# Optimization experiments

Measured on AMD Instinct MI355X. Metric: run time of the kernel, lower is better.

## Reference

```python
import jax, jax.numpy as jnp
import numpy as np

B, L, D_MODEL, D_STATE, D_CONV, EXPAND = 2, 1024, 1024, 16, 4, 2
D_INNER = D_MODEL * EXPAND


def setup_inputs() -> dict:
    key = jax.random.key(0)
    ks = jax.random.split(key, 8)
    s = lambda fan: 1.0 / np.sqrt(fan)
    x = jax.random.normal(ks[0], (B, L, D_MODEL), jnp.float32)
    in_proj_w = jax.random.normal(ks[1], (D_MODEL, 2 * D_INNER), jnp.float32) * s(D_MODEL)
    conv_w = jax.random.normal(ks[2], (D_INNER, 1, D_CONV), jnp.float32) * s(D_CONV)
    conv_b = jax.random.normal(ks[3], (D_INNER,), jnp.float32) * 0.01
    x_proj_w = jax.random.normal(ks[4], (D_INNER, 2 * D_STATE + D_INNER), jnp.float32) * s(D_INNER)
    dt_proj_w = jax.random.normal(ks[5], (D_INNER, D_INNER), jnp.float32) * s(D_INNER)
    dt_proj_b = jax.random.normal(ks[6], (D_INNER,), jnp.float32) * 0.01
    A_log = jnp.log(jnp.tile(jnp.arange(1, D_STATE + 1, dtype=jnp.float32)[None, :], (D_INNER, 1)))
    D = jnp.ones((D_INNER,), jnp.float32)
    out_proj_w = jax.random.normal(ks[7], (D_INNER, D_MODEL), jnp.float32) * s(D_INNER)
    return {"x": x, "in_proj_w": in_proj_w, "conv_w": conv_w, "conv_b": conv_b,
            "x_proj_w": x_proj_w, "dt_proj_w": dt_proj_w, "dt_proj_b": dt_proj_b,
            "A_log": A_log, "D": D, "out_proj_w": out_proj_w}


def _mamba_forward(x, in_proj_w, conv_w, conv_b, x_proj_w, dt_proj_w, dt_proj_b, A_log, D, out_proj_w):
    Bb, Ll, _ = x.shape
    d_inner, _, d_conv = conv_w.shape
    d_state = A_log.shape[1]
    # input projection and gate split
    xz = x @ in_proj_w                       # [B, L, 2*Di]
    x_inner, z = jnp.split(xz, 2, axis=-1)   # each [B, L, Di]
    # causal depthwise conv (left pad k-1, truncate to L == torch pad+slice)
    xc = jnp.transpose(x_inner, (0, 2, 1))   # [B, Di, L]
    xc = jax.lax.conv_general_dilated(
        xc, conv_w, window_strides=(1,), padding=[(d_conv - 1, 0)],
        dimension_numbers=("NCH", "OIH", "NCH"), feature_group_count=d_inner)
    xc = xc + conv_b[None, :, None]
    u = jax.nn.silu(jnp.transpose(xc, (0, 2, 1)))  # [B, L, Di]
    # SSM parameter projections
    ssm = u @ x_proj_w                        # [B, L, 2N+Di]
    B_ssm = ssm[..., :d_state]                # [B, L, N]
    C_ssm = ssm[..., d_state:2 * d_state]     # [B, L, N]
    dt = jax.nn.softplus(ssm[..., 2 * d_state:] @ dt_proj_w + dt_proj_b)  # [B, L, Di]
    A_real = -jnp.exp(A_log)                  # [Di, N]
    # selective scan over sequence (recurrence via lax.scan)
    def step(h, inp):
        dt_t, B_t, u_t = inp                  # [B,Di], [B,N], [B,Di]
        dA = jnp.exp(dt_t[..., None] * A_real)            # [B, Di, N]
        dBu = dt_t[..., None] * B_t[:, None, :] * u_t[..., None]
        h = dA * h + dBu
        return h, h
    h0 = jnp.zeros((Bb, d_inner, d_state), x.dtype)
    xs = (jnp.swapaxes(dt, 0, 1), jnp.swapaxes(B_ssm, 0, 1), jnp.swapaxes(u, 0, 1))
    _, states = jax.lax.scan(step, h0, xs)    # [L, B, Di, N]
    y = jnp.einsum("lbdn,lbn->lbd", states, jnp.swapaxes(C_ssm, 0, 1))
    y = jnp.swapaxes(y, 0, 1) + D * u         # skip connection
    y = y * jax.nn.silu(z)                    # gating
    return y @ out_proj_w                     # [B, L, d_model]


def reference(x, in_proj_w, conv_w, conv_b, x_proj_w, dt_proj_w, dt_proj_b, A_log, D, out_proj_w):
    return _mamba_forward(x, in_proj_w, conv_w, conv_b, x_proj_w, dt_proj_w, dt_proj_b, A_log, D, out_proj_w)
```

## Files before the change

kernel.cpp:

```cpp
#include <hip/hip_runtime.h>
#include <hip/hip_bf16.h>

#define BB 2
#define LL 1024
#define DMODEL 1024
#define DINNER 2048
#define DSTATE 16
#define DCONV 4
#define MM (BB * LL)
#define N_XZ 4096
#define N_SSM 2080
#define N_SSM_PAD 2176
#define CCH 32
#define LCH 32

typedef __hip_bfloat16 bf16;
typedef short bf16x8 __attribute__((ext_vector_type(8)));
typedef float f32x4 __attribute__((ext_vector_type(4)));

__device__ __forceinline__ void load16_lds(const bf16* g, bf16* l) {
    __builtin_amdgcn_global_load_lds(
        (const __attribute__((address_space(1))) void*)g,
        (__attribute__((address_space(3))) void*)l,
        16, 0, 0);
}

__global__ __launch_bounds__(256) void prep_kernel(
    const float* __restrict__ x, bf16* __restrict__ xbf,
    const float* __restrict__ w1, bf16* __restrict__ o1,
    const float* __restrict__ w2, bf16* __restrict__ o2,
    const float* __restrict__ w3, bf16* __restrict__ o3,
    const float* __restrict__ w4, bf16* __restrict__ o4)
{
    int bid = blockIdx.x;
    const float* src; bf16* dst; int K, N, tn, tk;
    if (bid < 4096)        { src = w1; dst = o1; K = 1024; N = 4096; tn = bid & 127; tk = bid >> 7; }
    else if (bid < 8256)   { bid -= 4096;  src = w2; dst = o2; K = 2048; N = 2080; tn = bid % 65; tk = bid / 65; }
    else if (bid < 12352)  { bid -= 8256;  src = w3; dst = o3; K = 2048; N = 2048; tn = bid & 63; tk = bid >> 6; }
    else if (bid < 14400)  { bid -= 12352; src = w4; dst = o4; K = 2048; N = 1024; tn = bid & 31; tk = bid >> 5; }
    else {
        bid -= 14400;
        int i = (bid * 256 + threadIdx.x) * 4;
        float4 v = *(const float4*)(x + i);
        xbf[i + 0] = __float2bfloat16(v.x);
        xbf[i + 1] = __float2bfloat16(v.y);
        xbf[i + 2] = __float2bfloat16(v.z);
        xbf[i + 3] = __float2bfloat16(v.w);
        return;
    }
    __shared__ float tile[32][33];
    const int nb = tn * 32, kb = tk * 32;
    const int tx = threadIdx.x & 31, ty = threadIdx.x >> 5;
    #pragma unroll
    for (int i = 0; i < 32; i += 8) {
        int k = kb + ty + i, n = nb + tx;
        tile[ty + i][tx] = (k < K && n < N) ? src[(size_t)k * N + n] : 0.f;
    }
    __syncthreads();
    #pragma unroll
    for (int i = 0; i < 32; i += 8) {
        int n = nb + ty + i, k = kb + tx;
        if (n < N && k < K) dst[(size_t)n * K + k] = __float2bfloat16(tile[tx][ty + i]);
    }
}

#define TM 128
#define TN 64
#define TK 64
template<int EPI, int KSPLIT = 1, int SWZ = -1>
__global__ __launch_bounds__(256) void mfma_gemm(
    const bf16* __restrict__ A, int lda,
    const bf16* __restrict__ Wt, int ldw,
    float* __restrict__ Cf, bf16* __restrict__ Cb, int ldc,
    const float* __restrict__ bias,
    int N, int K)
{
    __shared__ __align__(16) bf16 As[3][TM * TK];
    __shared__ __align__(16) bf16 Bs[3][TN * TK];
    const int tid = threadIdx.x;
    const int wave = tid >> 6, lane = tid & 63;
    const int wm = (wave >> 1) * 64, wn = (wave & 1) * 32;

    int bx, by;
    if (SWZ >= 0) {
        int id = blockIdx.x + (int)(gridDim.x * blockIdx.y);
        int xcd = id & 7, slot = id >> 3;
        bx = (xcd << SWZ) + (slot & ((1 << SWZ) - 1));
        by = slot >> SWZ;
    } else { bx = blockIdx.x; by = blockIdx.y; }
    const int m0 = by * TM, n0 = bx * TN;
    const int lm = lane & 15, kq = lane >> 4;

    const int srow = lane >> 3;
    const int schunk = (lane & 7) ^ srow;
    const bf16* gA = A + (size_t)(m0 + wave * 32 + srow) * lda + schunk * 8;
    const bf16* gB = Wt + (size_t)(n0 + wave * 16 + srow) * ldw + schunk * 8;

    const int Kc = K / KSPLIT;
    const int kbeg = (KSPLIT > 1) ? blockIdx.z * Kc : 0;
    const int NK = Kc / TK;

    f32x4 acc[4][2] = {};
    const int fsw = (lm & 7);

    auto stage = [&](int buf, int it) {
        const int k0 = kbeg + it * TK;
        bf16* lA = &As[buf][(wave * 32) * TK];
        bf16* lB = &Bs[buf][(wave * 16) * TK];
        #pragma unroll
        for (int g = 0; g < 4; ++g)
            load16_lds(gA + (size_t)(8 * g) * lda + k0, lA + (8 * g) * TK);
        #pragma unroll
        for (int g = 0; g < 2; ++g)
            load16_lds(gB + (size_t)(8 * g) * ldw + k0, lB + (8 * g) * TK);
    };
    auto compute = [&](int buf) {
        bf16x8 af[4][2], bfr[2][2];
        #pragma unroll
        for (int i = 0; i < 4; ++i)
            #pragma unroll
            for (int t = 0; t < 2; ++t)
                af[i][t] = *(const bf16x8*)(&As[buf][(wm + i * 16 + lm) * TK + ((t * 4 + kq) ^ fsw) * 8]);
        #pragma unroll
        for (int j = 0; j < 2; ++j)
            #pragma unroll
            for (int t = 0; t < 2; ++t)
                bfr[j][t] = *(const bf16x8*)(&Bs[buf][(wn + j * 16 + lm) * TK + ((t * 4 + kq) ^ fsw) * 8]);
        #pragma unroll
        for (int t = 0; t < 2; ++t)
            #pragma unroll
            for (int i = 0; i < 4; ++i)
                #pragma unroll
                for (int j = 0; j < 2; ++j)
                    acc[i][j] = __builtin_amdgcn_mfma_f32_16x16x32_bf16(af[i][t], bfr[j][t], acc[i][j], 0, 0, 0);
    };

    stage(0, 0); stage(1, 1); stage(2, 2);
    for (int it = 0; it < NK; ++it) {
        if (it + 2 < NK)      __builtin_amdgcn_s_waitcnt(0x0F7C);
        else if (it + 1 < NK) __builtin_amdgcn_s_waitcnt(0x0F76);
        else                  __builtin_amdgcn_s_waitcnt(0x0F70);
        __builtin_amdgcn_s_barrier();
        const int buf = it % 3;
        compute(buf);
        __builtin_amdgcn_s_barrier();
        if (it + 3 < NK) stage(buf, it + 3);
    }

    #pragma unroll
    for (int i = 0; i < 4; ++i) {
        #pragma unroll
        for (int j = 0; j < 2; ++j) {
            int gcol = n0 + wn + j * 16 + lm;
            if ((EPI == 0 || EPI == 3) && gcol >= N) continue;
            #pragma unroll
            for (int r = 0; r < 4; ++r) {
                int grow = m0 + wm + i * 16 + kq * 4 + r;
                float v = acc[i][j][r];
                if (EPI == 1) {
                    v += bias[gcol];
                    v = (v > 20.f) ? v : log1pf(__expf(v));
                    Cf[(size_t)grow * ldc + gcol] = v;
                } else if (EPI == 2) {
                    if (KSPLIT > 1) atomicAdd(&Cf[(size_t)grow * ldc + gcol], v);
                    else            Cf[(size_t)grow * ldc + gcol] = v;
                } else if (EPI == 3) {
                    if (gcol < 32) Cf[(size_t)grow * 32 + gcol] = v;
                    else           Cb[(size_t)grow * ldc + gcol] = __float2bfloat16(v);
                } else {
                    Cb[(size_t)grow * ldc + gcol] = __float2bfloat16(v);
                }
            }
        }
    }
}

__global__ void conv_silu_kernel(const bf16* __restrict__ xz,
                                 const float* __restrict__ conv_w,
                                 const float* __restrict__ conv_b,
                                 bf16* __restrict__ u)
{
    int idx = blockIdx.x * blockDim.x + threadIdx.x;
    int d8 = idx & (DINNER / 8 - 1);
    int l  = (idx >> 8) & (LL - 1);
    int b  = idx >> 18;
    int d0 = d8 * 8;

    float acc[8];
    {
        float4 b0 = *(const float4*)(conv_b + d0);
        float4 b1 = *(const float4*)(conv_b + d0 + 4);
        acc[0] = b0.x; acc[1] = b0.y; acc[2] = b0.z; acc[3] = b0.w;
        acc[4] = b1.x; acc[5] = b1.y; acc[6] = b1.z; acc[7] = b1.w;
    }
    #pragma unroll
    for (int j = 0; j < DCONV; ++j) {
        int ll = l - (DCONV - 1) + j;
        if (ll >= 0) {
            bf16x8 v = *(const bf16x8*)(xz + ((size_t)(b * LL + ll)) * N_XZ + d0);
            #pragma unroll
            for (int r = 0; r < 8; ++r) {
                float xv = __uint_as_float(((unsigned)(unsigned short)v[r]) << 16);
                acc[r] = fmaf(conv_w[(d0 + r) * DCONV + j], xv, acc[r]);
            }
        }
    }
    bf16x8 out;
    #pragma unroll
    for (int r = 0; r < 8; ++r) {
        float y = acc[r] / (1.f + __expf(-acc[r]));
        bf16 h = __float2bfloat16(y);
        out[r] = *reinterpret_cast<short*>(&h);
    }
    *(bf16x8*)(u + ((size_t)(b * LL + l)) * DINNER + d0) = out;
}

__global__ __launch_bounds__(256) void scan_phase_a(
    const float* __restrict__ dt, const bf16* __restrict__ u,
    const float* __restrict__ BC,
    const float* __restrict__ A_log,
    float* __restrict__ chunkP, float* __restrict__ chunkH)
{
    const int d = blockIdx.x * 256 + threadIdx.x;
    const int c = blockIdx.y, b = blockIdx.z;
    const int l0 = c * LCH;

    float A[DSTATE];
    {
        const f32x4* ap = (const f32x4*)(A_log + d * DSTATE);
        #pragma unroll
        for (int q = 0; q < 4; ++q) {
            f32x4 v = ap[q];
            #pragma unroll
            for (int r = 0; r < 4; ++r) A[q * 4 + r] = -__expf(v[r]);
        }
    }
    float h[DSTATE];
    #pragma unroll
    for (int n = 0; n < DSTATE; ++n) h[n] = 0.f;
    float sdt = 0.f;

    const float* dtp = dt + ((size_t)b * LL + l0) * DINNER + d;
    const bf16* up = u + ((size_t)b * LL + l0) * DINNER + d;
    const float* bcp = BC + ((size_t)b * LL + l0) * 32;

    #pragma unroll 2
    for (int i = 0; i < LCH; ++i) {
        float dtv = *dtp;
        float uv  = (float)*up;
        float du  = dtv * uv;
        f32x4 Bv[4];
        #pragma unroll
        for (int q = 0; q < 4; ++q) Bv[q] = *(const f32x4*)(bcp + q * 4);
        #pragma unroll
        for (int n = 0; n < DSTATE; ++n) {
            float a = __expf(dtv * A[n]);
            h[n] = fmaf(a, h[n], du * Bv[n >> 2][n & 3]);
        }
        sdt += dtv;
        dtp += DINNER; up += DINNER; bcp += 32;
    }

    size_t idx = (((size_t)b * CCH + c) * DINNER + d) * DSTATE;
    #pragma unroll
    for (int q = 0; q < 4; ++q) {
        f32x4 pv, hv;
        #pragma unroll
        for (int r = 0; r < 4; ++r) { pv[r] = __expf(A[q * 4 + r] * sdt); hv[r] = h[q * 4 + r]; }
        *(f32x4*)(chunkP + idx + q * 4) = pv;
        *(f32x4*)(chunkH + idx + q * 4) = hv;
    }
}

__global__ __launch_bounds__(256) void scan_phase_p(
    const float* __restrict__ chunkP, float* __restrict__ chunkH)
{
    int gid = blockIdx.x * 256 + threadIdx.x;
    int n = gid & 15;
    int d = (gid >> 4) & (DINNER - 1);
    int b = gid >> 15;
    const size_t stride = (size_t)DINNER * DSTATE;
    size_t idx = ((size_t)b * CCH * DINNER + d) * DSTATE + n;
    float H = 0.f;
    for (int c = 0; c < CCH; ++c) {
        float P  = chunkP[idx];
        float hl = chunkH[idx];
        chunkH[idx] = H;
        H = fmaf(P, H, hl);
        idx += stride;
    }
}

__global__ __launch_bounds__(256) void scan_phase_b(
    const float* __restrict__ dt, bf16* __restrict__ u,
    const float* __restrict__ BC, const bf16* __restrict__ xz,
    const float* __restrict__ A_log, const float* __restrict__ Dp,
    const float* __restrict__ chunkH)
{
    const int d = blockIdx.x * 256 + threadIdx.x;
    const int c = blockIdx.y, b = blockIdx.z;
    const int l0 = c * LCH;

    float A[DSTATE];
    {
        const f32x4* ap = (const f32x4*)(A_log + d * DSTATE);
        #pragma unroll
        for (int q = 0; q < 4; ++q) {
            f32x4 v = ap[q];
            #pragma unroll
            for (int r = 0; r < 4; ++r) A[q * 4 + r] = -__expf(v[r]);
        }
    }
    const float Dd = Dp[d];
    float h[DSTATE];
    {
        size_t idx = (((size_t)b * CCH + c) * DINNER + d) * DSTATE;
        #pragma unroll
        for (int q = 0; q < 4; ++q) {
            f32x4 v = *(const f32x4*)(chunkH + idx + q * 4);
            #pragma unroll
            for (int r = 0; r < 4; ++r) h[q * 4 + r] = v[r];
        }
    }

    const float* dtp = dt + ((size_t)b * LL + l0) * DINNER + d;
    bf16* up = u + ((size_t)b * LL + l0) * DINNER + d;
    const float* bcp = BC + ((size_t)b * LL + l0) * 32;
    const bf16* zp = xz + ((size_t)b * LL + l0) * N_XZ + DINNER + d;

    #pragma unroll 2
    for (int i = 0; i < LCH; ++i) {
        float dtv = *dtp;
        float uv  = (float)*up;
        float du  = dtv * uv;
        f32x4 Bv[4], Cv[4];
        #pragma unroll
        for (int q = 0; q < 4; ++q) {
            Bv[q] = *(const f32x4*)(bcp + q * 4);
            Cv[q] = *(const f32x4*)(bcp + 16 + q * 4);
        }
        float acc = 0.f;
        #pragma unroll
        for (int n = 0; n < DSTATE; ++n) {
            float a = __expf(dtv * A[n]);
            h[n] = fmaf(a, h[n], du * Bv[n >> 2][n & 3]);
            acc = fmaf(h[n], Cv[n >> 2][n & 3], acc);
        }
        float zv = (float)*zp;
        acc = fmaf(Dd, uv, acc);
        acc *= zv / (1.f + __expf(-zv));
        *up = __float2bfloat16(acc);
        dtp += DINNER; up += DINNER; bcp += 32; zp += N_XZ;
    }
}

extern "C" void kernel_launch(void* const* d_in, const int* in_sizes, int n_in,
                              void* d_out, int out_size, void* d_ws, size_t ws_size,
                              hipStream_t stream) {
    const float* x         = (const float*)d_in[0];
    const float* in_proj_w = (const float*)d_in[1];
    const float* conv_w    = (const float*)d_in[2];
    const float* conv_b    = (const float*)d_in[3];
    const float* x_proj_w  = (const float*)d_in[4];
    const float* dt_proj_w = (const float*)d_in[5];
    const float* dt_proj_b = (const float*)d_in[6];
    const float* A_log     = (const float*)d_in[7];
    const float* Dp        = (const float*)d_in[8];
    const float* out_proj_w= (const float*)d_in[9];
    float* out = (float*)d_out;

    char* p = (char*)d_ws;
    float* dt   = (float*)p;                          p += (size_t)MM * DINNER * 4;
    bf16*  xbf  = (bf16*)dt;
    bf16*  xz   = (bf16*)p;                           p += (size_t)MM * N_XZ * 2;
    bf16*  u    = (bf16*)p;                           p += (size_t)MM * DINNER * 2;
    bf16*  ssm  = (bf16*)p;                           p += (size_t)MM * N_SSM * 2;
    bf16*  Wt1  = (bf16*)p;                           p += (size_t)N_XZ * DMODEL * 2;
    bf16*  Wt2  = (bf16*)p;                           p += (size_t)N_SSM_PAD * DINNER * 2;
    bf16*  Wt3  = (bf16*)p;                           p += (size_t)DINNER * DINNER * 2;
    bf16*  Wt4  = (bf16*)p;                           p += (size_t)DMODEL * DINNER * 2;
    float* BC   = (float*)p;                          p += (size_t)MM * 32 * 4;
    float* chunkP = (float*)Wt1;
    float* chunkH = (float*)Wt2;

    prep_kernel<<<16448, 256, 0, stream>>>(x, xbf, in_proj_w, Wt1, x_proj_w, Wt2,
                                           dt_proj_w, Wt3, out_proj_w, Wt4);
    mfma_gemm<0, 1, 3><<<dim3(N_XZ / TN, MM / TM), 256, 0, stream>>>(
        xbf, DMODEL, Wt1, DMODEL, nullptr, xz, N_XZ, nullptr, N_XZ, DMODEL);
    {
        int n = BB * LL * DINNER / 8;
        conv_silu_kernel<<<(n + 255) / 256, 256, 0, stream>>>(xz, conv_w, conv_b, u);
    }
    mfma_gemm<3><<<dim3(N_SSM_PAD / TN, MM / TM), 256, 0, stream>>>(
        u, DINNER, Wt2, DINNER, BC, ssm, N_SSM, nullptr, N_SSM, DINNER);
    mfma_gemm<1, 1, 2><<<dim3(DINNER / TN, MM / TM), 256, 0, stream>>>(
        ssm + 2 * DSTATE, N_SSM, Wt3, DINNER, dt, nullptr, DINNER, dt_proj_b, DINNER, DINNER);
    scan_phase_a<<<dim3(DINNER / 256, CCH, BB), 256, 0, stream>>>(dt, u, BC, A_log, chunkP, chunkH);
    scan_phase_p<<<dim3(BB * DINNER * DSTATE / 256), 256, 0, stream>>>(chunkP, chunkH);
    scan_phase_b<<<dim3(DINNER / 256, CCH, BB), 256, 0, stream>>>(dt, u, BC, xz, A_log, Dp, chunkH);
    hipMemsetAsync(out, 0, (size_t)out_size * sizeof(float), stream);
    mfma_gemm<2, 2, 1><<<dim3(DMODEL / TN, MM / TM, 2), 256, 0, stream>>>(
        u, DINNER, Wt4, DINNER, out, nullptr, DMODEL, nullptr, DMODEL, DINNER);
}
```

Measured before the change: 363.4 us.

## Fold dt_proj into x_proj weights, fuse GEMMs into dual launches, double-buffer

Precomputes a fused weight W_x[:,32:] @ dt_proj_w in a dual-GEMM launch that runs alongside the in_proj GEMM. dt can then be computed directly from u in one GEMM, which removes the intermediate ssm projection. The B/C columns are computed by a small extra GEMM sharing the same launch. The pipeline also changes from triple- to double-buffered LDS, and the out_proj split-K goes from 2 to 4. This cuts one GEMM launch and the ssm round-trip at the cost of extra weight-product work each call and a changed rounding order for dt.

After: 334.2 us. -8.0%, faster.

```diff
diff --git a/kernel.cpp b/kernel.cpp
--- a/kernel.cpp
+++ b/kernel.cpp
@@ -28,18 +28,14 @@
 __global__ __launch_bounds__(256) void prep_kernel(
     const float* __restrict__ x, bf16* __restrict__ xbf,
     const float* __restrict__ w1, bf16* __restrict__ o1,
-    const float* __restrict__ w2, bf16* __restrict__ o2,
     const float* __restrict__ w3, bf16* __restrict__ o3,
-    const float* __restrict__ w4, bf16* __restrict__ o4)
+    const float* __restrict__ w4, bf16* __restrict__ o4,
+    const float* __restrict__ w2, bf16* __restrict__ w2bf,
+    bf16* __restrict__ w2bc)
 {
     int bid = blockIdx.x;
-    const float* src; bf16* dst; int K, N, tn, tk;
-    if (bid < 4096)        { src = w1; dst = o1; K = 1024; N = 4096; tn = bid & 127; tk = bid >> 7; }
-    else if (bid < 8256)   { bid -= 4096;  src = w2; dst = o2; K = 2048; N = 2080; tn = bid % 65; tk = bid / 65; }
-    else if (bid < 12352)  { bid -= 8256;  src = w3; dst = o3; K = 2048; N = 2048; tn = bid & 63; tk = bid >> 6; }
-    else if (bid < 14400)  { bid -= 12352; src = w4; dst = o4; K = 2048; N = 1024; tn = bid & 31; tk = bid >> 5; }
-    else {
-        bid -= 14400;
+    if (bid >= 14464) {
+        bid -= 14464;
         int i = (bid * 256 + threadIdx.x) * 4;
         float4 v = *(const float4*)(x + i);
         xbf[i + 0] = __float2bfloat16(v.x);
@@ -48,13 +44,28 @@
         xbf[i + 3] = __float2bfloat16(v.w);
         return;
     }
+    if (bid >= 10240 && bid < 14400) {
+        bid -= 10240;
+        int i = (bid * 256 + threadIdx.x) * 4;
+        float4 v = *(const float4*)(w2 + i);
+        w2bf[i + 0] = __float2bfloat16(v.x);
+        w2bf[i + 1] = __float2bfloat16(v.y);
+        w2bf[i + 2] = __float2bfloat16(v.z);
+        w2bf[i + 3] = __float2bfloat16(v.w);
+        return;
+    }
+    const float* src; bf16* dst; int K, N, tn, tk, srcld;
+    if (bid < 4096)        { src = w1; dst = o1; K = 1024; N = 4096; tn = bid & 127; tk = bid >> 7; srcld = N; }
+    else if (bid < 8192)   { bid -= 4096; src = w3; dst = o3; K = 2048; N = 2048; tn = bid & 63; tk = bid >> 6; srcld = N; }
+    else if (bid < 10240)  { bid -= 8192; src = w4; dst = o4; K = 2048; N = 1024; tn = bid & 31; tk = bid >> 5; srcld = N; }
+    else                   { bid -= 14400; src = w2; dst = w2bc; K = 2048; N = 32; tn = 0; tk = bid; srcld = N_SSM; }
     __shared__ float tile[32][33];
     const int nb = tn * 32, kb = tk * 32;
     const int tx = threadIdx.x & 31, ty = threadIdx.x >> 5;
     #pragma unroll
     for (int i = 0; i < 32; i += 8) {
         int k = kb + ty + i, n = nb + tx;
-        tile[ty + i][tx] = (k < K && n < N) ? src[(size_t)k * N + n] : 0.f;
+        tile[ty + i][tx] = (k < K && n < N) ? src[(size_t)k * srcld + n] : 0.f;
     }
     __syncthreads();
     #pragma unroll
@@ -67,27 +78,28 @@
 #define TM 128
 #define TN 64
 #define TK 64
-template<int EPI, int KSPLIT = 1, int SWZ = -1>
-__global__ __launch_bounds__(256) void mfma_gemm(
+
+template<int SWZ>
+__device__ __forceinline__ void remap(int id, int NX, int& bx, int& by) {
+    if (SWZ >= 0) {
+        int xcd = id & 7, slot = id >> 3;
+        bx = (xcd << SWZ) + (slot & ((1 << SWZ) - 1));
+        by = slot >> SWZ;
+    } else { bx = id % NX; by = id / NX; }
+}
+
+template<int EPI>
+__device__ __forceinline__ void gemm_body(
+    bf16* AsB, bf16* BsB, int bx, int by,
     const bf16* __restrict__ A, int lda,
     const bf16* __restrict__ Wt, int ldw,
     float* __restrict__ Cf, bf16* __restrict__ Cb, int ldc,
     const float* __restrict__ bias,
-    int N, int K)
-{
-    __shared__ __align__(16) bf16 As[3][TM * TK];
-    __shared__ __align__(16) bf16 Bs[3][TN * TK];
+    int N, int K, int kbeg, int Kc, bool at)
+{
     const int tid = threadIdx.x;
     const int wave = tid >> 6, lane = tid & 63;
     const int wm = (wave >> 1) * 64, wn = (wave & 1) * 32;
-
-    int bx, by;
-    if (SWZ >= 0) {
-        int id = blockIdx.x + (int)(gridDim.x * blockIdx.y);
-        int xcd = id & 7, slot = id >> 3;
-        bx = (xcd << SWZ) + (slot & ((1 << SWZ) - 1));
-        by = slot >> SWZ;
-    } else { bx = blockIdx.x; by = blockIdx.y; }
     const int m0 = by * TM, n0 = bx * TN;
     const int lm = lane & 15, kq = lane >> 4;
 
@@ -96,17 +108,14 @@
     const bf16* gA = A + (size_t)(m0 + wave * 32 + srow) * lda + schunk * 8;
     const bf16* gB = Wt + (size_t)(n0 + wave * 16 + srow) * ldw + schunk * 8;
 
-    const int Kc = K / KSPLIT;
-    const int kbeg = (KSPLIT > 1) ? blockIdx.z * Kc : 0;
     const int NK = Kc / TK;
-
     f32x4 acc[4][2] = {};
     const int fsw = (lm & 7);
 
     auto stage = [&](int buf, int it) {
         const int k0 = kbeg + it * TK;
-        bf16* lA = &As[buf][(wave * 32) * TK];
-        bf16* lB = &Bs[buf][(wave * 16) * TK];
+        bf16* lA = AsB + buf * (TM * TK) + (wave * 32) * TK;
+        bf16* lB = BsB + buf * (TN * TK) + (wave * 16) * TK;
         #pragma unroll
         for (int g = 0; g < 4; ++g)
             load16_lds(gA + (size_t)(8 * g) * lda + k0, lA + (8 * g) * TK);
@@ -115,17 +124,19 @@
             load16_lds(gB + (size_t)(8 * g) * ldw + k0, lB + (8 * g) * TK);
     };
     auto compute = [&](int buf) {
+        const bf16* Asb = AsB + buf * (TM * TK);
+        const bf16* Bsb = BsB + buf * (TN * TK);
         bf16x8 af[4][2], bfr[2][2];
         #pragma unroll
         for (int i = 0; i < 4; ++i)
             #pragma unroll
             for (int t = 0; t < 2; ++t)
-                af[i][t] = *(const bf16x8*)(&As[buf][(wm + i * 16 + lm) * TK + ((t * 4 + kq) ^ fsw) * 8]);
+                af[i][t] = *(const bf16x8*)(&Asb[(wm + i * 16 + lm) * TK + ((t * 4 + kq) ^ fsw) * 8]);
         #pragma unroll
         for (int j = 0; j < 2; ++j)
             #pragma unroll
             for (int t = 0; t < 2; ++t)
-                bfr[j][t] = *(const bf16x8*)(&Bs[buf][(wn + j * 16 + lm) * TK + ((t * 4 + kq) ^ fsw) * 8]);
+                bfr[j][t] = *(const bf16x8*)(&Bsb[(wn + j * 16 + lm) * TK + ((t * 4 + kq) ^ fsw) * 8]);
         #pragma unroll
         for (int t = 0; t < 2; ++t)
             #pragma unroll
@@ -135,16 +146,22 @@
                     acc[i][j] = __builtin_amdgcn_mfma_f32_16x16x32_bf16(af[i][t], bfr[j][t], acc[i][j], 0, 0, 0);
     };
 
-    stage(0, 0); stage(1, 1); stage(2, 2);
-    for (int it = 0; it < NK; ++it) {
-        if (it + 2 < NK)      __builtin_amdgcn_s_waitcnt(0x0F7C);
-        else if (it + 1 < NK) __builtin_amdgcn_s_waitcnt(0x0F76);
-        else                  __builtin_amdgcn_s_waitcnt(0x0F70);
+    stage(0, 0);
+    for (int it = 0; it < NK; it += 2) {
+        stage(1, it + 1);
+        __builtin_amdgcn_s_waitcnt(0x0F76);
         __builtin_amdgcn_s_barrier();
-        const int buf = it % 3;
-        compute(buf);
+        compute(0);
         __builtin_amdgcn_s_barrier();
-        if (it + 3 < NK) stage(buf, it + 3);
+        if (it + 2 < NK) {
+            stage(0, it + 2);
+            __builtin_amdgcn_s_waitcnt(0x0F76);
+        } else {
+            __builtin_amdgcn_s_waitcnt(0x0F70);
+        }
+        __builtin_amdgcn_s_barrier();
+        compute(1);
+        __builtin_amdgcn_s_barrier();
     }
 
     #pragma unroll
@@ -162,8 +179,8 @@
                     v = (v > 20.f) ? v : log1pf(__expf(v));
                     Cf[(size_t)grow * ldc + gcol] = v;
                 } else if (EPI == 2) {
-                    if (KSPLIT > 1) atomicAdd(&Cf[(size_t)grow * ldc + gcol], v);
-                    else            Cf[(size_t)grow * ldc + gcol] = v;
+                    if (at) atomicAdd(&Cf[(size_t)grow * ldc + gcol], v);
+                    else    Cf[(size_t)grow * ldc + gcol] = v;
                 } else if (EPI == 3) {
                     if (gcol < 32) Cf[(size_t)grow * 32 + gcol] = v;
                     else           Cb[(size_t)grow * ldc + gcol] = __float2bfloat16(v);
@@ -172,6 +189,53 @@
                 }
             }
         }
+    }
+}
+
+template<int EPI, int KSPLIT = 1, int SWZ = -1>
+__global__ __launch_bounds__(256) void mfma_gemm(
+    const bf16* __restrict__ A, int lda,
+    const bf16* __restrict__ Wt, int ldw,
+    float* __restrict__ Cf, bf16* __restrict__ Cb, int ldc,
+    const float* __restrict__ bias,
+    int N, int K)
+{
+    __shared__ __align__(16) bf16 As[2][TM * TK];
+    __shared__ __align__(16) bf16 Bs[2][TN * TK];
+    int bx, by;
+    if (SWZ >= 0) {
+        int id = blockIdx.x + (int)(gridDim.x * blockIdx.y);
+        remap<SWZ>(id, gridDim.x, bx, by);
+    } else { bx = blockIdx.x; by = blockIdx.y; }
+    const int Kc = K / KSPLIT;
+    const int kbeg = (KSPLIT > 1) ? blockIdx.z * Kc : 0;
+    gemm_body<EPI>(&As[0][0], &Bs[0][0], bx, by, A, lda, Wt, ldw, Cf, Cb, ldc,
+                   bias, N, K, kbeg, Kc, KSPLIT > 1);
+}
+
+template<int EPI0, int SWZ0, int EPI1, int SWZ1>
+__global__ __launch_bounds__(256) void mfma_gemm_dual(
+    int nblk0, int NX0,
+    const bf16* __restrict__ A0, int lda0, const bf16* __restrict__ Wt0, int ldw0,
+    float* __restrict__ Cf0, bf16* __restrict__ Cb0, int ldc0,
+    const float* __restrict__ bias0, int N0, int K0,
+    int NX1,
+    const bf16* __restrict__ A1, int lda1, const bf16* __restrict__ Wt1, int ldw1,
+    float* __restrict__ Cf1, bf16* __restrict__ Cb1, int ldc1,
+    const float* __restrict__ bias1, int N1, int K1)
+{
+    __shared__ __align__(16) bf16 As[2][TM * TK];
+    __shared__ __align__(16) bf16 Bs[2][TN * TK];
+    int id = blockIdx.x;
+    if (id < nblk0) {
+        int bx, by; remap<SWZ0>(id, NX0, bx, by);
+        gemm_body<EPI0>(&As[0][0], &Bs[0][0], bx, by, A0, lda0, Wt0, ldw0,
+                        Cf0, Cb0, ldc0, bias0, N0, K0, 0, K0, false);
+    } else {
+        id -= nblk0;
+        int bx, by; remap<SWZ1>(id, NX1, bx, by);
+        gemm_body<EPI1>(&As[0][0], &Bs[0][0], bx, by, A1, lda1, Wt1, ldw1,
+                        Cf1, Cb1, ldc1, bias1, N1, K1, 0, K1, false);
     }
 }
 
@@ -374,31 +438,33 @@
     bf16*  xbf  = (bf16*)dt;
     bf16*  xz   = (bf16*)p;                           p += (size_t)MM * N_XZ * 2;
     bf16*  u    = (bf16*)p;                           p += (size_t)MM * DINNER * 2;
-    bf16*  ssm  = (bf16*)p;                           p += (size_t)MM * N_SSM * 2;
+    bf16*  wft  = (bf16*)p;                           p += (size_t)MM * N_SSM * 2;
     bf16*  Wt1  = (bf16*)p;                           p += (size_t)N_XZ * DMODEL * 2;
-    bf16*  Wt2  = (bf16*)p;                           p += (size_t)N_SSM_PAD * DINNER * 2;
+    bf16*  w2slot = (bf16*)p;                         p += (size_t)N_SSM_PAD * DINNER * 2;
+    bf16*  W2bf = w2slot;
+    bf16*  w2bc = w2slot + (size_t)DINNER * N_SSM;
     bf16*  Wt3  = (bf16*)p;                           p += (size_t)DINNER * DINNER * 2;
     bf16*  Wt4  = (bf16*)p;                           p += (size_t)DMODEL * DINNER * 2;
     float* BC   = (float*)p;                          p += (size_t)MM * 32 * 4;
     float* chunkP = (float*)Wt1;
-    float* chunkH = (float*)Wt2;
-
-    prep_kernel<<<16448, 256, 0, stream>>>(x, xbf, in_proj_w, Wt1, x_proj_w, Wt2,
-                                           dt_proj_w, Wt3, out_proj_w, Wt4);
-    mfma_gemm<0, 1, 3><<<dim3(N_XZ / TN, MM / TM), 256, 0, stream>>>(
-        xbf, DMODEL, Wt1, DMODEL, nullptr, xz, N_XZ, nullptr, N_XZ, DMODEL);
+    float* chunkH = (float*)w2slot;
+
+    prep_kernel<<<16512, 256, 0, stream>>>(x, xbf, in_proj_w, Wt1, dt_proj_w, Wt3,
+                                           out_proj_w, Wt4, x_proj_w, W2bf, w2bc);
+    mfma_gemm_dual<0, 3, 0, 2><<<1536, 256, 0, stream>>>(
+        1024, 64, xbf, DMODEL, Wt1, DMODEL, nullptr, xz, N_XZ, nullptr, N_XZ, DMODEL,
+        32, Wt3, DINNER, W2bf + 32, N_SSM, nullptr, wft, DINNER, nullptr, DINNER, DINNER);
     {
         int n = BB * LL * DINNER / 8;
         conv_silu_kernel<<<(n + 255) / 256, 256, 0, stream>>>(xz, conv_w, conv_b, u);
     }
-    mfma_gemm<3><<<dim3(N_SSM_PAD / TN, MM / TM), 256, 0, stream>>>(
-        u, DINNER, Wt2, DINNER, BC, ssm, N_SSM, nullptr, N_SSM, DINNER);
-    mfma_gemm<1, 1, 2><<<dim3(DINNER / TN, MM / TM), 256, 0, stream>>>(
-        ssm + 2 * DSTATE, N_SSM, Wt3, DINNER, dt, nullptr, DINNER, dt_proj_b, DINNER, DINNER);
+    mfma_gemm_dual<1, 2, 3, -1><<<528, 256, 0, stream>>>(
+        512, 32, u, DINNER, wft, DINNER, dt, nullptr, DINNER, dt_proj_b, DINNER, DINNER,
+        1, u, DINNER, w2bc, DINNER, BC, nullptr, 32, nullptr, 32, DINNER);
     scan_phase_a<<<dim3(DINNER / 256, CCH, BB), 256, 0, stream>>>(dt, u, BC, A_log, chunkP, chunkH);
     scan_phase_p<<<dim3(BB * DINNER * DSTATE / 256), 256, 0, stream>>>(chunkP, chunkH);
     scan_phase_b<<<dim3(DINNER / 256, CCH, BB), 256, 0, stream>>>(dt, u, BC, xz, A_log, Dp, chunkH);
     hipMemsetAsync(out, 0, (size_t)out_size * sizeof(float), stream);
-    mfma_gemm<2, 2, 1><<<dim3(DMODEL / TN, MM / TM, 2), 256, 0, stream>>>(
+    mfma_gemm<2, 4, 1><<<dim3(DMODEL / TN, MM / TM, 4), 256, 0, stream>>>(
         u, DINNER, Wt4, DINNER, out, nullptr, DMODEL, nullptr, DMODEL, DINNER);
 }
```
